# Kernel optimization log

Measured on AMD Instinct MI355X. Metric: run time of the kernel, lower is better.

Reference implementation:

```python
import jax, jax.numpy as jnp
import numpy as np

N_NODES = 100000
N_EDGES = 3200000
N_GRAPHS = 1024


def _gcn_norm(edge_index, num_nodes):
    # PyG GCNConv: add self-loops, symmetric normalization D^-1/2 (A+I) D^-1/2
    src, dst = edge_index[0], edge_index[1]
    loop = jnp.arange(num_nodes, dtype=edge_index.dtype)
    src = jnp.concatenate([src, loop])
    dst = jnp.concatenate([dst, loop])
    ones = jnp.ones(src.shape[0], dtype=jnp.float32)
    deg = jax.ops.segment_sum(ones, dst, num_segments=num_nodes)
    dinv = jnp.where(deg > 0, jax.lax.rsqrt(deg), 0.0)
    norm = dinv[src] * dinv[dst]  # [E+N]
    return src, dst, norm


def _gcn_conv(x, W, b, src, dst, norm, num_nodes):
    h = x @ W                              # [N, out]
    msgs = h[src] * norm[:, None]          # gather + scale  [E+N, out]
    agg = jax.ops.segment_sum(msgs, dst, num_segments=num_nodes)
    return agg + b


def setup_inputs() -> dict:
    key = jax.random.key(0)
    ks = jax.random.split(key, 8)
    x = jax.random.normal(ks[0], (N_NODES, 5), dtype=jnp.float32)
    edge_index = jax.random.randint(ks[1], (2, N_EDGES), 0, N_NODES, dtype=jnp.int64)
    batch = jnp.sort(jax.random.randint(ks[2], (N_NODES,), 0, N_GRAPHS, dtype=jnp.int64))
    # Glorot-ish init for GCN weights, like PyG defaults
    W1 = jax.random.normal(ks[3], (5, 16), dtype=jnp.float32) * (1.0 / np.sqrt(5))
    b1 = jnp.zeros((16,), dtype=jnp.float32)
    W2 = jax.random.normal(ks[4], (16, 32), dtype=jnp.float32) * (1.0 / np.sqrt(16))
    b2 = jnp.zeros((32,), dtype=jnp.float32)
    fcW = jax.random.normal(ks[5], (32, 1), dtype=jnp.float32) * (1.0 / np.sqrt(32))
    fcb = jnp.zeros((1,), dtype=jnp.float32)
    return {"x": x, "edge_index": edge_index, "batch": batch,
            "W1": W1, "b1": b1, "W2": W2, "b2": b2, "fcW": fcW, "fcb": fcb}


def reference(x, edge_index, batch, W1, b1, W2, b2, fcW, fcb):
    src, dst, norm = _gcn_norm(edge_index, N_NODES)
    h = jax.nn.relu(_gcn_conv(x, W1, b1, src, dst, norm, N_NODES))
    h = jax.nn.relu(_gcn_conv(h, W2, b2, src, dst, norm, N_NODES))
    # global_mean_pool over batch ids
    sums = jax.ops.segment_sum(h, batch, num_segments=N_GRAPHS)
    cnts = jax.ops.segment_sum(jnp.ones((h.shape[0],), dtype=h.dtype), batch,
                               num_segments=N_GRAPHS)
    pooled = sums / jnp.maximum(cnts, 1.0)[:, None]   # [G, 32]
    return pooled @ fcW + fcb                          # [G, 1]
```

## Files before the change

### kernel.cpp

```cpp
#include <hip/hip_runtime.h>
#include <hip/hip_fp16.h>


#define RANGE 256
#define NB 391
#define RPB (RANGE + 1)
#define CAP 10240
#define NBLK 512
#define CHUNKMAX 6400
#define PSPREAD 8

__global__ void k_cnt(const int* __restrict__ dst, int E, int chunk,
                      int* __restrict__ blkcnt) {
    __shared__ int h[NB];
    for (int t = threadIdx.x; t < NB; t += blockDim.x) h[t] = 0;
    __syncthreads();
    int e0 = blockIdx.x * chunk;
    int e1 = min(e0 + chunk, E);
    for (int e = e0 + threadIdx.x; e < e1; e += blockDim.x)
        atomicAdd(&h[dst[e] >> 8], 1);
    __syncthreads();
    int* row = blkcnt + (size_t)blockIdx.x * NB;
    for (int t = threadIdx.x; t < NB; t += blockDim.x) row[t] = h[t];
}

__global__ __launch_bounds__(512) void k_scanb(const int* __restrict__ blkcnt,
        int* __restrict__ base, int* __restrict__ bfill) {
    __shared__ int part[NBLK];
    int b = blockIdx.x, t = threadIdx.x;
    int v = blkcnt[(size_t)t * NB + b];
    part[t] = v;
    __syncthreads();
    for (int off = 1; off < NBLK; off <<= 1) {
        int u = (t >= off) ? part[t - off] : 0;
        __syncthreads();
        part[t] += u;
        __syncthreads();
    }
    base[(size_t)b * NBLK + t] = b * CAP + part[t] - v;
    if (t == NBLK - 1) bfill[b] = part[t];
}

__global__ __launch_bounds__(512) void k_scat(const int* __restrict__ src,
        const int* __restrict__ dst, int E, int chunk,
        const int* __restrict__ base, unsigned int* __restrict__ recbuf) {
    __shared__ unsigned int lbuf[CHUNKMAX];
    __shared__ unsigned short bkt[CHUNKMAX];
    __shared__ int h[NB], lsc[NB], h2[NB], base_l[NB];
    __shared__ int sc[512];
    int t = threadIdx.x;
    if (t < NB) { h[t] = 0; h2[t] = 0; }
    __syncthreads();
    int e0 = blockIdx.x * chunk;
    int e1 = min(e0 + chunk, E);
    int len = e1 - e0;
    for (int e = e0 + t; e < e1; e += 512)
        atomicAdd(&h[__builtin_nontemporal_load(dst + e) >> 8], 1);
    __syncthreads();
    int v = (t < NB) ? h[t] : 0;
    sc[t] = v;
    __syncthreads();
    for (int off = 1; off < 512; off <<= 1) {
        int u = (t >= off) ? sc[t - off] : 0;
        __syncthreads();
        sc[t] += u;
        __syncthreads();
    }
    if (t < NB) {
        lsc[t] = sc[t] - v;
        base_l[t] = base[(size_t)t * NBLK + blockIdx.x];
    }
    __syncthreads();
    for (int e = e0 + t; e < e1; e += 512) {
        int d = __builtin_nontemporal_load(dst + e);
        int s = __builtin_nontemporal_load(src + e);
        int b = d >> 8;
        int r = atomicAdd(&h2[b], 1);
        int pos = lsc[b] + r;
        lbuf[pos] = ((unsigned)s << 8) | (unsigned)(d & 255);
        bkt[pos] = (unsigned short)b;
    }
    __syncthreads();
    for (int i = t; i < len; i += 512) {
        int b = bkt[i];
        recbuf[base_l[b] + (i - lsc[b])] = lbuf[i];
    }
}

__global__ __launch_bounds__(512) void k_sort(const int* __restrict__ bfill,
        const unsigned int* __restrict__ recbuf, int* __restrict__ rowp,
        int* __restrict__ srt, const float* __restrict__ x,
        float* __restrict__ dinv, float* __restrict__ sx8, int N) {
    __shared__ int cnt[RANGE], lbase[RANGE], rank[RANGE], sc[RANGE];
    int b = blockIdx.x;
    int t = threadIdx.x;
    if (t < RANGE) { cnt[t] = 0; rank[t] = 0; }
    __syncthreads();
    int len = bfill[b];
    int g0 = b * CAP;
    const unsigned* rb = recbuf + (size_t)g0;
    for (int r = t; r < len; r += 512)
        atomicAdd(&cnt[__builtin_nontemporal_load(rb + r) & 255], 1);
    __syncthreads();
    if (t < RANGE) sc[t] = cnt[t];
    __syncthreads();
    for (int off = 1; off < RANGE; off <<= 1) {
        int u = 0;
        if (t < RANGE && t >= off) u = sc[t - off];
        __syncthreads();
        if (t < RANGE) sc[t] += u;
        __syncthreads();
    }
    if (t < RANGE) {
        lbase[t] = sc[t] - cnt[t];
        rowp[b * RPB + t] = g0 + lbase[t];
        if (t == RANGE - 1) rowp[b * RPB + RANGE] = g0 + sc[t];
        int i = b * RANGE + t;
        if (i < N) {
            float di = rsqrtf((float)(cnt[t] + 1));
            dinv[i] = di;
            float4 a, bb;
            a.x = x[i * 5 + 0] * di; a.y = x[i * 5 + 1] * di;
            a.z = x[i * 5 + 2] * di; a.w = x[i * 5 + 3] * di;
            bb.x = x[i * 5 + 4] * di; bb.y = 0.f; bb.z = 0.f; bb.w = 0.f;
            float4* p = (float4*)(sx8 + (size_t)i * 8);
            p[0] = a; p[1] = bb;
        }
    }
    __syncthreads();
    for (int r = t; r < len; r += 512) {
        unsigned rec = __builtin_nontemporal_load(rb + r);
        int key = (int)(rec & 255);
        int pos = g0 + lbase[key] + atomicAdd(&rank[key], 1);
        srt[pos] = (int)(rec >> 8);
    }
}

__global__ void k_gather8(const int* __restrict__ rowp, const int* __restrict__ srt,
                          const float* __restrict__ sx8, float* __restrict__ agg8, int N) {
    int wid = (blockIdx.x * blockDim.x + threadIdx.x) >> 6;
    int lane = threadIdx.x & 63;
    if (wid >= N) return;
    int k = lane & 7, j = lane >> 3;
    int b = wid >> 8, dl = wid & 255;
    int base = b * RPB + dl;
    int p0 = rowp[base], p1 = rowp[base + 1];
    float acc = 0.f;
    int p = p0 + j;
    while (p < p1) {
        int s0 = __builtin_nontemporal_load(srt + p);
        int s1 = __builtin_nontemporal_load(srt + p + 8);
        int s2 = __builtin_nontemporal_load(srt + p + 16);
        int s3 = __builtin_nontemporal_load(srt + p + 24);
        int s4 = __builtin_nontemporal_load(srt + p + 32);
        int s5 = __builtin_nontemporal_load(srt + p + 40);
        int s6 = __builtin_nontemporal_load(srt + p + 48);
        int s7 = __builtin_nontemporal_load(srt + p + 56);
        s1 = (p + 8  < p1) ? s1 : N;
        s2 = (p + 16 < p1) ? s2 : N;
        s3 = (p + 24 < p1) ? s3 : N;
        s4 = (p + 32 < p1) ? s4 : N;
        s5 = (p + 40 < p1) ? s5 : N;
        s6 = (p + 48 < p1) ? s6 : N;
        s7 = (p + 56 < p1) ? s7 : N;
        float v0 = sx8[(size_t)s0 * 8 + k];
        float v1 = sx8[(size_t)s1 * 8 + k];
        float v2 = sx8[(size_t)s2 * 8 + k];
        float v3 = sx8[(size_t)s3 * 8 + k];
        float v4 = sx8[(size_t)s4 * 8 + k];
        float v5 = sx8[(size_t)s5 * 8 + k];
        float v6 = sx8[(size_t)s6 * 8 + k];
        float v7 = sx8[(size_t)s7 * 8 + k];
        acc += ((v0 + v1) + (v2 + v3)) + ((v4 + v5) + (v6 + v7));
        p += 64;
    }
    acc += __shfl_xor(acc, 8, 64);
    acc += __shfl_xor(acc, 16, 64);
    acc += __shfl_xor(acc, 32, 64);
    if (lane < 8) agg8[(size_t)wid * 8 + k] = acc + sx8[(size_t)wid * 8 + k];
}

__global__ void k_lin1(const float* __restrict__ agg8, const float* __restrict__ dinv,
                       const float* __restrict__ W1, const float* __restrict__ b1,
                       __half* __restrict__ g, int N) {
    __shared__ float sW[80], sb[16];
    if (threadIdx.x < 80) sW[threadIdx.x] = W1[threadIdx.x];
    if (threadIdx.x < 16) sb[threadIdx.x] = b1[threadIdx.x];
    __syncthreads();
    int i = blockIdx.x * blockDim.x + threadIdx.x;
    if (i > N) return;
    uint4* gp = (uint4*)(g + (size_t)i * 16);
    if (i == N) {
        uint4 z = {0u, 0u, 0u, 0u};
        gp[0] = z; gp[1] = z;
        return;
    }
    float di = dinv[i];
    const float4* a4 = (const float4*)(agg8 + (size_t)i * 8);
    float4 v0 = a4[0], v1 = a4[1];
    float a[5] = {v0.x, v0.y, v0.z, v0.w, v1.x};
    union { __half h[16]; uint4 u[2]; } pk;
#pragma unroll
    for (int kk = 0; kk < 16; ++kk) {
        float h = 0.f;
#pragma unroll
        for (int d = 0; d < 5; ++d) h = fmaf(a[d], sW[d * 16 + kk], h);
        h = fmaxf(fmaf(di, h, sb[kk]), 0.f);
        pk.h[kk] = __float2half(h * di);
    }
    gp[0] = pk.u[0];
    gp[1] = pk.u[1];
}

__global__ void k_gather16(const int* __restrict__ rowp, const int* __restrict__ srt,
                           const __half* __restrict__ g, float* __restrict__ agg16, int N) {
    int wid = (blockIdx.x * blockDim.x + threadIdx.x) >> 6;
    int lane = threadIdx.x & 63;
    if (wid >= N) return;
    int k = lane & 7, j = lane >> 3;
    int b = wid >> 8, dl = wid & 255;
    int base = b * RPB + dl;
    int p0 = rowp[base], p1 = rowp[base + 1];
    const __half2* gp = (const __half2*)g;
    float ax = 0.f, ay = 0.f;
    int p = p0 + j;
    while (p < p1) {
        int s0 = __builtin_nontemporal_load(srt + p);
        int s1 = __builtin_nontemporal_load(srt + p + 8);
        int s2 = __builtin_nontemporal_load(srt + p + 16);
        int s3 = __builtin_nontemporal_load(srt + p + 24);
        int s4 = __builtin_nontemporal_load(srt + p + 32);
        int s5 = __builtin_nontemporal_load(srt + p + 40);
        int s6 = __builtin_nontemporal_load(srt + p + 48);
        int s7 = __builtin_nontemporal_load(srt + p + 56);
        s1 = (p + 8  < p1) ? s1 : N;
        s2 = (p + 16 < p1) ? s2 : N;
        s3 = (p + 24 < p1) ? s3 : N;
        s4 = (p + 32 < p1) ? s4 : N;
        s5 = (p + 40 < p1) ? s5 : N;
        s6 = (p + 48 < p1) ? s6 : N;
        s7 = (p + 56 < p1) ? s7 : N;
        __half2 h0 = gp[(size_t)s0 * 8 + k];
        __half2 h1 = gp[(size_t)s1 * 8 + k];
        __half2 h2 = gp[(size_t)s2 * 8 + k];
        __half2 h3 = gp[(size_t)s3 * 8 + k];
        __half2 h4 = gp[(size_t)s4 * 8 + k];
        __half2 h5 = gp[(size_t)s5 * 8 + k];
        __half2 h6 = gp[(size_t)s6 * 8 + k];
        __half2 h7 = gp[(size_t)s7 * 8 + k];
        float2 f0 = __half22float2(h0);
        float2 f1 = __half22float2(h1);
        float2 f2 = __half22float2(h2);
        float2 f3 = __half22float2(h3);
        float2 f4 = __half22float2(h4);
        float2 f5 = __half22float2(h5);
        float2 f6 = __half22float2(h6);
        float2 f7 = __half22float2(h7);
        ax += ((f0.x + f1.x) + (f2.x + f3.x)) + ((f4.x + f5.x) + (f6.x + f7.x));
        ay += ((f0.y + f1.y) + (f2.y + f3.y)) + ((f4.y + f5.y) + (f6.y + f7.y));
        p += 64;
    }
    ax += __shfl_xor(ax, 8, 64);
    ax += __shfl_xor(ax, 16, 64);
    ax += __shfl_xor(ax, 32, 64);
    ay += __shfl_xor(ay, 8, 64);
    ay += __shfl_xor(ay, 16, 64);
    ay += __shfl_xor(ay, 32, 64);
    if (lane < 8) {
        float2 self = __half22float2(gp[(size_t)wid * 8 + k]);
        agg16[(size_t)wid * 16 + 2 * k]     = ax + self.x;
        agg16[(size_t)wid * 16 + 2 * k + 1] = ay + self.y;
    }
}

__global__ void k_fin(const float* __restrict__ agg16, const float* __restrict__ dinv,
                      const float* __restrict__ W2, const float* __restrict__ b2,
                      const float* __restrict__ fcW, const int* __restrict__ batch,
                      float* __restrict__ pool, int* __restrict__ gcnt, int N, int G) {
    __shared__ float sW[512], sb[32], sf[32];
    for (int t = threadIdx.x; t < 512; t += blockDim.x) sW[t] = W2[t];
    if (threadIdx.x < 32) {
        sb[threadIdx.x] = b2[threadIdx.x];
        sf[threadIdx.x] = fcW[threadIdx.x];
    }
    __syncthreads();
    int i = blockIdx.x * blockDim.x + threadIdx.x;
    if (i >= N) return;
    float di = dinv[i];
    float a[16];
    const float4* a4 = (const float4*)(agg16 + (size_t)i * 16);
#pragma unroll
    for (int q = 0; q < 4; ++q) {
        float4 v = a4[q];
        a[q * 4 + 0] = v.x; a[q * 4 + 1] = v.y; a[q * 4 + 2] = v.z; a[q * 4 + 3] = v.w;
    }
    float c = 0.f;
#pragma unroll
    for (int jj = 0; jj < 32; ++jj) {
        float acc2 = 0.f;
#pragma unroll
        for (int kk = 0; kk < 16; ++kk) acc2 = fmaf(a[kk], sW[kk * 32 + jj], acc2);
        float h = fmaxf(fmaf(di, acc2, sb[jj]), 0.f);
        c = fmaf(h, sf[jj], c);
    }
    int bidx = batch[i];
    int slot = i & (PSPREAD - 1);
    atomicAdd(&pool[slot * G + bidx], c);
    atomicAdd(&gcnt[slot * G + bidx], 1);
}

__global__ void k_out(const float* __restrict__ pool, const int* __restrict__ gcnt,
                      const float* __restrict__ fcb, float* __restrict__ out, int G) {
    int gI = blockIdx.x * blockDim.x + threadIdx.x;
    if (gI >= G) return;
    float s = 0.f; int c = 0;
#pragma unroll
    for (int k = 0; k < PSPREAD; ++k) { s += pool[k * G + gI]; c += gcnt[k * G + gI]; }
    out[gI] = s / fmaxf((float)c, 1.f) + fcb[0];
}

extern "C" void kernel_launch(void* const* d_in, const int* in_sizes, int n_in,
                              void* d_out, int out_size, void* d_ws, size_t ws_size,
                              hipStream_t stream) {
    const float* x    = (const float*)d_in[0];
    const int*   ei   = (const int*)d_in[1];
    const int*   batch= (const int*)d_in[2];
    const float* W1   = (const float*)d_in[3];
    const float* b1   = (const float*)d_in[4];
    const float* W2   = (const float*)d_in[5];
    const float* b2   = (const float*)d_in[6];
    const float* fcW  = (const float*)d_in[7];
    const float* fcb  = (const float*)d_in[8];
    float* out = (float*)d_out;

    const int N = in_sizes[0] / 5;
    const int E = in_sizes[1] / 2;
    const int G = out_size;
    const int chunk = (E + NBLK - 1) / NBLK;

    const int* src = ei;
    const int* dst = ei + E;

    char* ws = (char*)d_ws;
    size_t o = 0;
    auto carve = [&](size_t bytes) -> char* {
        char* p = ws + o;
        o += (bytes + 255) & ~(size_t)255;
        return p;
    };
    int*   bfill   = (int*)carve((size_t)4 * NB);
    int*   rowp    = (int*)carve((size_t)4 * (NB * RPB + 4));
    float* dinv    = (float*)carve((size_t)4 * N);
    float* sx8     = (float*)carve((size_t)32 * (N + 1));
    float* agg8    = (float*)carve((size_t)32 * N);
    int*   srt     = (int*)carve((size_t)4 * NB * CAP + 256);
    char*  rbase   = carve((size_t)4 * NB * CAP);
    int*   blkcnt  = srt;
    int*   base    = srt + (size_t)NBLK * NB;
    unsigned int* recbuf = (unsigned int*)rbase;
    __half* g      = (__half*)rbase;
    float* agg16   = (float*)(rbase + (((size_t)32 * (N + 1) + 255) & ~(size_t)255));
    float* pool    = (float*)carve((size_t)4 * PSPREAD * G);
    int*   gcnt    = (int*)carve((size_t)4 * PSPREAD * G);

    hipMemsetAsync(pool, 0, (size_t)8 * PSPREAD * G, stream);
    hipMemsetAsync(sx8 + (size_t)8 * N, 0, 32, stream);

    k_cnt<<<NBLK, 256, 0, stream>>>(dst, E, chunk, blkcnt);
    k_scanb<<<NB, 512, 0, stream>>>(blkcnt, base, bfill);
    k_scat<<<NBLK, 512, 0, stream>>>(src, dst, E, chunk, base, recbuf);
    k_sort<<<NB, 512, 0, stream>>>(bfill, recbuf, rowp, srt, x, dinv, sx8, N);
    {
        int blocks = (int)(((long long)N * 64 + 255) / 256);
        k_gather8<<<blocks, 256, 0, stream>>>(rowp, srt, sx8, agg8, N);
    }
    k_lin1<<<(N + 256) / 256, 256, 0, stream>>>(agg8, dinv, W1, b1, g, N);
    {
        int blocks = (int)(((long long)N * 64 + 255) / 256);
        k_gather16<<<blocks, 256, 0, stream>>>(rowp, srt, g, agg16, N);
    }
    k_fin<<<(N + 255) / 256, 256, 0, stream>>>(agg16, dinv, W2, b2, fcW, batch, pool, gcnt, N, G);
    k_out<<<(G + 255) / 256, 256, 0, stream>>>(pool, gcnt, fcb, out, G);
}
```

Measured before the change: 166.8 us.

## Store scaled input features as fp16 for first gather and fold memsets into kernels

The dinv-scaled input feature table used by the first aggregation is stored as packed fp16 (16 bytes per node instead of 32), and the gather kernel now reads half2 pairs with 4 lanes per row and 16 edges in flight per wave iteration. The two hipMemsetAsync calls are removed: pool/gcnt zeroing moves into k_cnt and the sentinel row zeroing moves into k_sort. This halves gather traffic for layer 1 and removes two launches, at the cost of fp16 rounding of the input features.

```diff
diff --git a/kernel.cpp b/kernel.cpp
--- a/kernel.cpp
+++ b/kernel.cpp
@@ -11,7 +11,9 @@
 #define PSPREAD 8
 
 __global__ void k_cnt(const int* __restrict__ dst, int E, int chunk,
-                      int* __restrict__ blkcnt) {
+                      int* __restrict__ blkcnt, int* __restrict__ poolgc, int nz) {
+    int z = blockIdx.x * blockDim.x + threadIdx.x;
+    if (z < nz) poolgc[z] = 0;
     __shared__ int h[NB];
     for (int t = threadIdx.x; t < NB; t += blockDim.x) h[t] = 0;
     __syncthreads();
@@ -90,11 +92,15 @@
 __global__ __launch_bounds__(512) void k_sort(const int* __restrict__ bfill,
         const unsigned int* __restrict__ recbuf, int* __restrict__ rowp,
         int* __restrict__ srt, const float* __restrict__ x,
-        float* __restrict__ dinv, float* __restrict__ sx8, int N) {
+        float* __restrict__ dinv, __half* __restrict__ sx8, int N) {
     __shared__ int cnt[RANGE], lbase[RANGE], rank[RANGE], sc[RANGE];
     int b = blockIdx.x;
     int t = threadIdx.x;
     if (t < RANGE) { cnt[t] = 0; rank[t] = 0; }
+    if (b == 0 && t == 0) {
+        uint4 z = {0u, 0u, 0u, 0u};
+        *(uint4*)(sx8 + (size_t)N * 8) = z;
+    }
     __syncthreads();
     int len = bfill[b];
     int g0 = b * CAP;
@@ -119,12 +125,11 @@
         if (i < N) {
             float di = rsqrtf((float)(cnt[t] + 1));
             dinv[i] = di;
-            float4 a, bb;
-            a.x = x[i * 5 + 0] * di; a.y = x[i * 5 + 1] * di;
-            a.z = x[i * 5 + 2] * di; a.w = x[i * 5 + 3] * di;
-            bb.x = x[i * 5 + 4] * di; bb.y = 0.f; bb.z = 0.f; bb.w = 0.f;
-            float4* p = (float4*)(sx8 + (size_t)i * 8);
-            p[0] = a; p[1] = bb;
+            union { __half h[8]; uint4 u; } pk;
+#pragma unroll
+            for (int d = 0; d < 5; ++d) pk.h[d] = __float2half(x[i * 5 + d] * di);
+            pk.h[5] = __float2half(0.f); pk.h[6] = __float2half(0.f); pk.h[7] = __float2half(0.f);
+            *(uint4*)(sx8 + (size_t)i * 8) = pk.u;
         }
     }
     __syncthreads();
@@ -137,47 +142,50 @@
 }
 
 __global__ void k_gather8(const int* __restrict__ rowp, const int* __restrict__ srt,
-                          const float* __restrict__ sx8, float* __restrict__ agg8, int N) {
+                          const __half* __restrict__ sx8, float* __restrict__ agg8, int N) {
     int wid = (blockIdx.x * blockDim.x + threadIdx.x) >> 6;
     int lane = threadIdx.x & 63;
     if (wid >= N) return;
-    int k = lane & 7, j = lane >> 3;
+    int k2 = lane & 3, j = lane >> 2;
     int b = wid >> 8, dl = wid & 255;
     int base = b * RPB + dl;
     int p0 = rowp[base], p1 = rowp[base + 1];
-    float acc = 0.f;
+    const __half2* tab = (const __half2*)sx8;
+    float ax = 0.f, ay = 0.f;
     int p = p0 + j;
     while (p < p1) {
         int s0 = __builtin_nontemporal_load(srt + p);
-        int s1 = __builtin_nontemporal_load(srt + p + 8);
-        int s2 = __builtin_nontemporal_load(srt + p + 16);
-        int s3 = __builtin_nontemporal_load(srt + p + 24);
-        int s4 = __builtin_nontemporal_load(srt + p + 32);
-        int s5 = __builtin_nontemporal_load(srt + p + 40);
-        int s6 = __builtin_nontemporal_load(srt + p + 48);
-        int s7 = __builtin_nontemporal_load(srt + p + 56);
-        s1 = (p + 8  < p1) ? s1 : N;
-        s2 = (p + 16 < p1) ? s2 : N;
-        s3 = (p + 24 < p1) ? s3 : N;
-        s4 = (p + 32 < p1) ? s4 : N;
-        s5 = (p + 40 < p1) ? s5 : N;
-        s6 = (p + 48 < p1) ? s6 : N;
-        s7 = (p + 56 < p1) ? s7 : N;
-        float v0 = sx8[(size_t)s0 * 8 + k];
-        float v1 = sx8[(size_t)s1 * 8 + k];
-        float v2 = sx8[(size_t)s2 * 8 + k];
-        float v3 = sx8[(size_t)s3 * 8 + k];
-        float v4 = sx8[(size_t)s4 * 8 + k];
-        float v5 = sx8[(size_t)s5 * 8 + k];
-        float v6 = sx8[(size_t)s6 * 8 + k];
-        float v7 = sx8[(size_t)s7 * 8 + k];
-        acc += ((v0 + v1) + (v2 + v3)) + ((v4 + v5) + (v6 + v7));
+        int s1 = __builtin_nontemporal_load(srt + p + 16);
+        int s2 = __builtin_nontemporal_load(srt + p + 32);
+        int s3 = __builtin_nontemporal_load(srt + p + 48);
+        s1 = (p + 16 < p1) ? s1 : N;
+        s2 = (p + 32 < p1) ? s2 : N;
+        s3 = (p + 48 < p1) ? s3 : N;
+        __half2 h0 = tab[(size_t)s0 * 4 + k2];
+        __half2 h1 = tab[(size_t)s1 * 4 + k2];
+        __half2 h2 = tab[(size_t)s2 * 4 + k2];
+        __half2 h3 = tab[(size_t)s3 * 4 + k2];
+        float2 f0 = __half22float2(h0);
+        float2 f1 = __half22float2(h1);
+        float2 f2 = __half22float2(h2);
+        float2 f3 = __half22float2(h3);
+        ax += (f0.x + f1.x) + (f2.x + f3.x);
+        ay += (f0.y + f1.y) + (f2.y + f3.y);
         p += 64;
     }
-    acc += __shfl_xor(acc, 8, 64);
-    acc += __shfl_xor(acc, 16, 64);
-    acc += __shfl_xor(acc, 32, 64);
-    if (lane < 8) agg8[(size_t)wid * 8 + k] = acc + sx8[(size_t)wid * 8 + k];
+    ax += __shfl_xor(ax, 4, 64);
+    ax += __shfl_xor(ax, 8, 64);
+    ax += __shfl_xor(ax, 16, 64);
+    ax += __shfl_xor(ax, 32, 64);
+    ay += __shfl_xor(ay, 4, 64);
+    ay += __shfl_xor(ay, 8, 64);
+    ay += __shfl_xor(ay, 16, 64);
+    ay += __shfl_xor(ay, 32, 64);
+    if (lane < 4) {
+        float2 self = __half22float2(tab[(size_t)wid * 4 + k2]);
+        agg8[(size_t)wid * 8 + 2 * k2]     = ax + self.x;
+        agg8[(size_t)wid * 8 + 2 * k2 + 1] = ay + self.y;
+    }
 }
 
 __global__ void k_lin1(const float* __restrict__ agg8, const float* __restrict__ dinv,
@@ -348,25 +356,24 @@
         o += (bytes + 255) & ~(size_t)255;
         return p;
     };
-    int*   bfill   = (int*)carve((size_t)4 * NB);
-    int*   rowp    = (int*)carve((size_t)4 * (NB * RPB + 4));
-    float* dinv    = (float*)carve((size_t)4 * N);
-    float* sx8     = (float*)carve((size_t)32 * (N + 1));
-    float* agg8    = (float*)carve((size_t)32 * N);
-    int*   srt     = (int*)carve((size_t)4 * NB * CAP + 256);
-    char*  rbase   = carve((size_t)4 * NB * CAP);
-    int*   blkcnt  = srt;
-    int*   base    = srt + (size_t)NBLK * NB;
+    int*    bfill   = (int*)carve((size_t)4 * NB);
+    int*    rowp    = (int*)carve((size_t)4 * (NB * RPB + 4));
+    float*  dinv    = (float*)carve((size_t)4 * N);
+    __half* sx8     = (__half*)carve((size_t)16 * (N + 1));
+    float*  agg8    = (float*)carve((size_t)32 * N);
+    int*    srt     = (int*)carve((size_t)4 * NB * CAP + 256);
+    char*   rbase   = carve((size_t)4 * NB * CAP);
+    int*    blkcnt  = srt;
+    int*    base    = srt + (size_t)NBLK * NB;
     unsigned int* recbuf = (unsigned int*)rbase;
-    __half* g      = (__half*)rbase;
-    float* agg16   = (float*)(rbase + (((size_t)32 * (N + 1) + 255) & ~(size_t)255));
-    float* pool    = (float*)carve((size_t)4 * PSPREAD * G);
-    int*   gcnt    = (int*)carve((size_t)4 * PSPREAD * G);
-
-    hipMemsetAsync(pool, 0, (size_t)8 * PSPREAD * G, stream);
-    hipMemsetAsync(sx8 + (size_t)8 * N, 0, 32, stream);
-
-    k_cnt<<<NBLK, 256, 0, stream>>>(dst, E, chunk, blkcnt);
+    __half* g       = (__half*)rbase;
+    float*  agg16   = (float*)(rbase + (((size_t)32 * (N + 1) + 255) & ~(size_t)255));
+    float*  pool    = (float*)carve((size_t)4 * PSPREAD * G);
+    int*    gcnt    = (int*)carve((size_t)4 * PSPREAD * G);
+
+    const int nz = 2 * PSPREAD * G;
+
+    k_cnt<<<NBLK, 256, 0, stream>>>(dst, E, chunk, blkcnt, (int*)pool, nz);
     k_scanb<<<NB, 512, 0, stream>>>(blkcnt, base, bfill);
     k_scat<<<NBLK, 512, 0, stream>>>(src, dst, E, chunk, base, recbuf);
     k_sort<<<NB, 512, 0, stream>>>(bfill, recbuf, rowp, srt, x, dinv, sx8, N);
```

New measurement: 156.1 us. 1.07x faster.
